# Optimization experiments

Hardware: AMD Instinct MI355X
Metric: run time of the kernel (lower is better)

Reference implementation:

```python
import jax, jax.numpy as jnp
import numpy as np

N_NODES = 4_000_000   # numNodes in the morphological tree
K_ATTRS = 6           # attributes per group
H = W = 4096          # image size
BETA_F = 100.0        # sigmoid gain (init kwarg)
N_DOUBLE = 22         # ceil(log2(N_NODES)) pointer-doubling steps


def setup_inputs() -> dict:
    key = jax.random.key(0)
    k1, k2, k3 = jax.random.split(key, 3)
    rng = np.random.default_rng(0)

    attrs2d = jax.random.uniform(k1, (N_NODES, K_ATTRS), dtype=jnp.float32)
    weight = jax.random.normal(k2, (K_ATTRS,), dtype=jnp.float32) * 0.5
    bias = jnp.zeros((1,), dtype=jnp.float32)
    # per-node gray-level residue (increment w.r.t. parent), non-negative for a max-tree
    residue = jax.random.uniform(k3, (N_NODES,), dtype=jnp.float32)

    # parent pointers: parent[i] < i (nodes in topological order), root 0 -> dummy node N
    par = np.empty(N_NODES + 1, dtype=np.int32)
    par[0] = N_NODES                       # root points at dummy
    idx = np.arange(1, N_NODES)
    par[1:N_NODES] = (rng.random(N_NODES - 1) * idx).astype(np.int32)
    par[N_NODES] = N_NODES                 # dummy is its own parent (value 0)
    parent = jnp.asarray(par)

    pixel_to_node = jnp.asarray(
        rng.integers(0, N_NODES, size=(H * W,), dtype=np.int32))

    return {"attrs2d": attrs2d, "weight": weight, "bias": bias,
            "residue": residue, "parent": parent, "pixel_to_node": pixel_to_node}


def _connected_filter(gate, residue, parent, pixel_to_node):
    """Soft connected filtering: y(p) = sum over root->node(p) path of gate*residue."""
    # append dummy node with value 0 at index N_NODES
    vals = jnp.concatenate([gate * residue, jnp.zeros((1,), gate.dtype)])  # (N+1,)
    cum, ptr = vals, parent
    for _ in range(N_DOUBLE):  # pointer doubling over the parent chain
        cum = cum + cum[ptr]
        ptr = ptr[ptr]
    return cum[pixel_to_node].reshape(H, W)


def reference(attrs2d, weight, bias, residue, parent, pixel_to_node):
    # logits = A @ w + b ; s = clamp(beta_f * logits, +-12) ; gate = sigmoid(s)
    logits = attrs2d @ weight + bias[0]                 # (N,)
    s = jnp.clip(BETA_F * logits, -12.0, 12.0)
    gate = jax.nn.sigmoid(s)
    return _connected_filter(gate, residue, parent, pixel_to_node)  # (H, W)
```

## Files before the change

### kernel.cpp

```cpp
#include <hip/hip_runtime.h>
#include <hip/hip_bf16.h>


typedef float v2f __attribute__((ext_vector_type(2)));
typedef float v4f __attribute__((ext_vector_type(4)));
typedef int   v4i __attribute__((ext_vector_type(4)));

#define NB 512
#define CHUNK_PX 8192
#define CV4 2048

__global__ __launch_bounds__(256) void k_gate_count512(
        const float* __restrict__ attrs, const float* __restrict__ w,
        const float* __restrict__ bias, const float* __restrict__ residue,
        const int* __restrict__ parent, int2* __restrict__ packed, int N,
        const int* __restrict__ ptn, unsigned short* __restrict__ wcnt,
        int shift, int g1) {
    __shared__ int hist[NB];
    if ((int)blockIdx.x >= g1) {
        int chunk = blockIdx.x - g1;
        int tid = threadIdx.x;
        for (int i = tid; i < NB; i += 256) hist[i] = 0;
        __syncthreads();
        const v4i* p4 = reinterpret_cast<const v4i*>(ptn) + (size_t)chunk * CV4;
        for (int t = 0; t < CV4/256; ++t) {
            v4i ia = __builtin_nontemporal_load(p4 + t*256 + tid);
            atomicAdd(&hist[ia.x >> shift], 1);
            atomicAdd(&hist[ia.y >> shift], 1);
            atomicAdd(&hist[ia.z >> shift], 1);
            atomicAdd(&hist[ia.w >> shift], 1);
        }
        __syncthreads();
        unsigned short* wc = wcnt + (size_t)chunk * NB;
        for (int i = tid; i < NB; i += 256) wc[i] = (unsigned short)hist[i];
        return;
    }
    int i = blockIdx.x * blockDim.x + threadIdx.x;
    if (i > N) return;
    if (i == N) { int2 p; p.x = N; p.y = __float_as_int(0.0f); packed[N] = p; return; }
    const v2f* a2 = reinterpret_cast<const v2f*>(attrs + (size_t)i * 6);
    v2f a0  = __builtin_nontemporal_load(a2 + 0);
    v2f a1  = __builtin_nontemporal_load(a2 + 1);
    v2f a2v = __builtin_nontemporal_load(a2 + 2);
    float logit = bias[0]
                + a0.x  * w[0] + a0.y  * w[1]
                + a1.x  * w[2] + a1.y  * w[3]
                + a2v.x * w[4] + a2v.y * w[5];
    float s = fminf(fmaxf(100.0f * logit, -12.0f), 12.0f);
    float gate = 1.0f / (1.0f + __expf(-s));
    float vv = gate * __builtin_nontemporal_load(residue + i);
    int2 p; p.x = __builtin_nontemporal_load(parent + i); p.y = __float_as_int(vv);
    packed[i] = p;
}

__global__ __launch_bounds__(512) void k_scanA(const unsigned short* __restrict__ wcnt,
                                               int* __restrict__ P) {
    int g = blockIdx.x, b = threadIdx.x;
    const unsigned short* base = wcnt + (size_t)g * 32 * NB;
    int s = 0;
    for (int i = 0; i < 32; ++i) s += base[(size_t)i*NB + b];
    P[(size_t)g*NB + b] = s;
}

__global__ __launch_bounds__(512) void k_scanB(int* __restrict__ P,
                                               int* __restrict__ binStart,
                                               int* __restrict__ binCnt, int nGroups) {
    int b = threadIdx.x, lane = b & 63, wave = b >> 6;
    int tot = 0;
    for (int g = 0; g < nGroups; ++g) {
        int t = P[(size_t)g*NB + b]; P[(size_t)g*NB + b] = tot; tot += t;
    }
    binCnt[b] = tot;
    int pad = (tot + 63) & ~63;
    int inc = pad;
    #pragma unroll
    for (int d = 1; d < 64; d <<= 1) { int o = __shfl_up(inc, d); if (lane >= d) inc += o; }
    __shared__ int wsum[8];
    if (lane == 63) wsum[wave] = inc;
    __syncthreads();
    int wb = 0;
    for (int ww = 0; ww < wave; ++ww) wb += wsum[ww];
    binStart[b] = wb + inc - pad;
}

__global__ __launch_bounds__(512) void k_scanC(const unsigned short* __restrict__ wcnt,
                                               const int* __restrict__ P,
                                               const int* __restrict__ binStart,
                                               int* __restrict__ bases) {
    int g = blockIdx.x, b = threadIdx.x;
    int run = binStart[b] + P[(size_t)g*NB + b];
    for (int i = 0; i < 32; ++i) {
        size_t c = (size_t)g*32 + i;
        bases[c*NB + b] = run;
        run += wcnt[c*NB + b];
    }
}

__global__ void k_walk_lvl0(const int2* __restrict__ packed,
                            float* __restrict__ cum, int hi, int N) {
    int i = blockIdx.x * blockDim.x + threadIdx.x;
    if (i >= hi) return;
    float s = 0.0f; int j = i;
    while (j != N) { int2 pv = packed[j]; s += __int_as_float(pv.y); j = pv.x; }
    cum[i] = s;
}

__global__ void k_walk_lvl(const int2* __restrict__ packed,
                           float* __restrict__ cum, int lo, int hi, int cutoff) {
    int i = lo + blockIdx.x * blockDim.x + threadIdx.x;
    if (i >= hi) return;
    float s = 0.0f; int j = i;
    do { int2 pv = packed[j]; s += __int_as_float(pv.y); j = pv.x; } while (j >= cutoff);
    cum[i] = s + cum[j];
}

__device__ __forceinline__ void exscan_bins(int* __restrict__ cnt,
                                            int* __restrict__ chEx,
                                            int* __restrict__ wsum) {
    int tid = threadIdx.x, lane = tid & 63, wave = tid >> 6;
    int b0 = 2*tid;
    int s0 = cnt[b0], s1 = cnt[b0+1], s = s0 + s1;
    int inc = s;
    #pragma unroll
    for (int d = 1; d < 64; d <<= 1) { int o = __shfl_up(inc, d); if (lane >= d) inc += o; }
    if (lane == 63) wsum[wave] = inc;
    __syncthreads();
    int wb = 0;
    for (int ww = 0; ww < wave; ++ww) wb += wsum[ww];
    int ex = wb + inc - s;
    chEx[b0] = ex; chEx[b0+1] = ex + s0;
}

__global__ __launch_bounds__(256) void k_scatter512(
        const int* __restrict__ ptn, const unsigned short* __restrict__ wcnt,
        const int* __restrict__ bases, int* __restrict__ nv,
        unsigned short* __restrict__ slotLocal, int shift) {
    __shared__ int cnt[NB];
    __shared__ int chEx[NB];
    __shared__ int alloc[NB];
    __shared__ int sbase[NB];
    __shared__ int ldss[CHUNK_PX];
    __shared__ int wsum[4];
    int chunk = blockIdx.x;
    int tid = threadIdx.x;
    const unsigned short* wc = wcnt + (size_t)chunk * NB;
    const int* bs = bases + (size_t)chunk * NB;
    for (int i = tid; i < NB; i += 256) { cnt[i] = wc[i]; sbase[i] = bs[i]; }
    __syncthreads();
    exscan_bins(cnt, chEx, wsum);
    __syncthreads();
    for (int i = tid; i < NB; i += 256) alloc[i] = chEx[i];
    __syncthreads();
    const v4i* p4 = reinterpret_cast<const v4i*>(ptn) + (size_t)chunk * CV4;
    unsigned long long* sl8 = reinterpret_cast<unsigned long long*>(slotLocal)
                              + (size_t)chunk * CV4;
    for (int t = 0; t < CV4/256; ++t) {
        v4i ia = __builtin_nontemporal_load(p4 + t*256 + tid);
        int s0 = atomicAdd(&alloc[ia.x >> shift], 1);
        int s1 = atomicAdd(&alloc[ia.y >> shift], 1);
        int s2 = atomicAdd(&alloc[ia.z >> shift], 1);
        int s3 = atomicAdd(&alloc[ia.w >> shift], 1);
        ldss[s0] = ia.x; ldss[s1] = ia.y; ldss[s2] = ia.z; ldss[s3] = ia.w;
        unsigned long long pk = (unsigned long long)(unsigned)s0
                              | ((unsigned long long)(unsigned)s1 << 16)
                              | ((unsigned long long)(unsigned)s2 << 32)
                              | ((unsigned long long)(unsigned)s3 << 48);
        sl8[t*256 + tid] = pk;
    }
    __syncthreads();
    {
        int grp = tid >> 4;
        int l16 = tid & 15;
        for (int b = grp; b < NB; b += 16) {
            int st = chEx[b], n = cnt[b], dst = sbase[b];
            for (int i = l16; i < n; i += 16)
                nv[dst + i] = ldss[st + i];
        }
    }
}

__global__ __launch_bounds__(512) void k_gather512(
        int* __restrict__ nv, const float* __restrict__ cum,
        const int* __restrict__ binStart, const int* __restrict__ binCnt,
        int shift, int N) {
    __shared__ float slice[8192];
    int b = blockIdx.x;
    int base = b << shift;
    int W = 1 << shift;
    for (int i = threadIdx.x; i < W; i += 512) {
        int idx = base + i;
        slice[i] = (idx < N) ? cum[idx] : 0.0f;
    }
    __syncthreads();
    int s = binStart[b], cnt = binCnt[b];
    int nq = cnt >> 2;
    v4i* np = reinterpret_cast<v4i*>(nv + s);
    v4f* vp = reinterpret_cast<v4f*>(nv + s);
    for (int q = threadIdx.x; q < nq; q += 512) {
        v4i na = __builtin_nontemporal_load(np + q);
        v4f va;
        va.x = slice[na.x - base];
        va.y = slice[na.y - base];
        va.z = slice[na.z - base];
        va.w = slice[na.w - base];
        vp[q] = va;
    }
    int r = cnt & 3;
    if ((int)threadIdx.x < r) {
        int i = s + nq*4 + threadIdx.x;
        float v = slice[nv[i] - base];
        reinterpret_cast<float*>(nv)[i] = v;
    }
}

__global__ __launch_bounds__(256) void k_merge512(
        const unsigned short* __restrict__ wcnt, const int* __restrict__ bases,
        const float* __restrict__ nvf, const unsigned short* __restrict__ slotLocal,
        float* __restrict__ out) {
    __shared__ int cnt[NB];
    __shared__ int chEx[NB + 1];
    __shared__ int sbase[NB];
    __shared__ float ldsv[CHUNK_PX];
    __shared__ int wsum[4];
    int chunk = blockIdx.x;
    int tid = threadIdx.x;
    const unsigned short* wc = wcnt + (size_t)chunk * NB;
    const int* bs = bases + (size_t)chunk * NB;
    for (int i = tid; i < NB; i += 256) { cnt[i] = wc[i]; sbase[i] = bs[i]; }
    __syncthreads();
    exscan_bins(cnt, chEx, wsum);
    if (tid == 0) chEx[NB] = CHUNK_PX;
    __syncthreads();
    {
        int grp = tid >> 4;
        int l16 = tid & 15;
        for (int b = grp; b < NB; b += 16) {
            int st = chEx[b], n = cnt[b], src = sbase[b];
            for (int i = l16; i < n; i += 16)
                ldsv[st + i] = nvf[src + i];
        }
    }
    __syncthreads();
    const unsigned long long* sl8 = reinterpret_cast<const unsigned long long*>(slotLocal)
                                    + (size_t)chunk * CV4;
    v4f* o4 = reinterpret_cast<v4f*>(out) + (size_t)chunk * CV4;
    for (int t = 0; t < CV4/256; ++t) {
        unsigned long long pk = __builtin_nontemporal_load(sl8 + t*256 + tid);
        v4f o;
        o.x = ldsv[pk & 0xFFFF];
        o.y = ldsv[(pk >> 16) & 0xFFFF];
        o.z = ldsv[(pk >> 32) & 0xFFFF];
        o.w = ldsv[(pk >> 48) & 0xFFFF];
        o4[t*256 + tid] = o;
    }
}

__global__ void k_pixel_gather(const float* __restrict__ cum,
                               const int* __restrict__ ptn,
                               float* __restrict__ out, int M) {
    int t = blockIdx.x * blockDim.x + threadIdx.x;
    int base = t * 4;
    if (base + 3 < M) {
        v4i idx = __builtin_nontemporal_load(reinterpret_cast<const v4i*>(ptn) + t);
        float4 o;
        o.x = cum[idx.x]; o.y = cum[idx.y]; o.z = cum[idx.z]; o.w = cum[idx.w];
        reinterpret_cast<float4*>(out)[t] = o;
    } else {
        for (int p = base; p < M; ++p) out[p] = cum[ptn[p]];
    }
}

extern "C" void kernel_launch(void* const* d_in, const int* in_sizes, int n_in,
                              void* d_out, int out_size, void* d_ws, size_t ws_size,
                              hipStream_t stream) {
    const float* attrs   = (const float*)d_in[0];
    const float* weight  = (const float*)d_in[1];
    const float* bias    = (const float*)d_in[2];
    const float* residue = (const float*)d_in[3];
    const int*   parent  = (const int*)d_in[4];
    const int*   ptn     = (const int*)d_in[5];
    float* out = (float*)d_out;

    const int N  = in_sizes[3];
    const int HW = in_sizes[5];
    const int BLK = 256;

    int shift = 0;
    while (((long)(N - 1) >> shift) >= NB) ++shift;
    int nBins = (int)(((long)(N - 1) >> shift) + 1);

    const int nChunks = HW / CHUNK_PX;
    const int nGroups = nChunks / 32;

    auto align256 = [](size_t x) { return (x + 255) & ~(size_t)255; };
    const size_t cumB   = align256((size_t)(N + 1) * 4);
    const size_t pkB    = (size_t)(N + 1) * 8;
    const size_t slB    = (size_t)HW * 2;
    const size_t regA   = align256(pkB > slB ? pkB : slB);
    const size_t nvB    = align256(((size_t)HW + (size_t)NB*64) * 4);
    const size_t wcntB  = align256((size_t)nChunks * NB * 2);
    const size_t PB     = align256((size_t)nGroups * NB * 4);
    const size_t basesB = align256((size_t)nChunks * NB * 4);
    const size_t need   = cumB + regA + nvB + wcntB + PB + basesB + 4096;

    float* cum    = (float*)d_ws;
    int2*  packed = (int2*)((char*)d_ws + cumB);
    unsigned short* slotLocal = (unsigned short*)((char*)d_ws + cumB);
    int*   nv     = (int*)((char*)d_ws + cumB + regA);
    unsigned short* wcnt = (unsigned short*)((char*)d_ws + cumB + regA + nvB);
    int*   P      = (int*)((char*)d_ws + cumB + regA + nvB + wcntB);
    int*   bases  = (int*)((char*)d_ws + cumB + regA + nvB + wcntB + PB);
    int*   binStart = (int*)((char*)d_ws + cumB + regA + nvB + wcntB + PB + basesB);
    int*   binCnt   = binStart + NB;

    bool binnedOK = (HW % CHUNK_PX == 0) && (nChunks % 32 == 0) && (nChunks >= 32) &&
                    (shift <= 13) && (ws_size >= need) && (N >= 2);

    int g1 = (N + 1 + BLK - 1) / BLK;
    int gC = binnedOK ? nChunks : 0;
    k_gate_count512<<<g1 + gC, BLK, 0, stream>>>(attrs, weight, bias, residue,
                                                 parent, packed, N,
                                                 ptn, wcnt, shift, g1);

    if (binnedOK) {
        k_scanA<<<nGroups, 512, 0, stream>>>(wcnt, P);
        k_scanB<<<1, 512, 0, stream>>>(P, binStart, binCnt, nGroups);
        k_scanC<<<nGroups, 512, 0, stream>>>(wcnt, P, binStart, bases);
    }

    int c0 = 16384;   if (c0 > N) c0 = N;
    int c1 = 262144;  if (c1 > N) c1 = N;
    int c2 = 1048576; if (c2 > N) c2 = N;

    k_walk_lvl0<<<(c0 + BLK - 1) / BLK, BLK, 0, stream>>>(packed, cum, c0, N);
    if (c1 > c0)
        k_walk_lvl<<<(c1 - c0 + BLK - 1) / BLK, BLK, 0, stream>>>(packed, cum, c0, c1, c0);
    if (c2 > c1)
        k_walk_lvl<<<(c2 - c1 + BLK - 1) / BLK, BLK, 0, stream>>>(packed, cum, c1, c2, c1);
    if (N > c2)
        k_walk_lvl<<<(N - c2 + BLK - 1) / BLK, BLK, 0, stream>>>(packed, cum, c2, N, c2);

    if (binnedOK) {
        k_scatter512<<<nChunks, BLK, 0, stream>>>(ptn, wcnt, bases, nv, slotLocal, shift);
        k_gather512<<<nBins, 512, 0, stream>>>(nv, cum, binStart, binCnt, shift, N);
        k_merge512<<<nChunks, BLK, 0, stream>>>(wcnt, bases, (const float*)nv,
                                                slotLocal, out);
    } else {
        int nQuads = (HW + 3) / 4;
        k_pixel_gather<<<(nQuads + BLK - 1) / BLK, BLK, 0, stream>>>(cum, ptn, out, HW);
    }
}
```

Baseline: 320.9 us.

## Interleave last-level tree walk with pixel scatter in one fused launch

The final pointer-walk level and the pixel scatter now run in a single interleaved kernel whose blocks alternate between scatter chunks and walk blocks. This lets the latency-bound walk overlap with the bandwidth-bound scatter instead of running them back to back. To make that safe, slotLocal moves to its own workspace region, because it previously aliased the packed buffer the walk reads. Chunk size is halved (4096 pixels) to double the number of chunks, and the bin-copy loops switch to 8-lane groups. Smaller chunks mean more per-chunk histogram and scan overhead and more, shorter bin runs.

```diff
diff --git a/kernel.cpp b/kernel.cpp
--- a/kernel.cpp
+++ b/kernel.cpp
@@ -7,8 +7,8 @@
 typedef int   v4i __attribute__((ext_vector_type(4)));
 
 #define NB 512
-#define CHUNK_PX 8192
-#define CV4 2048
+#define CHUNK_PX 4096
+#define CV4 1024
 
 __global__ __launch_bounds__(256) void k_gate_count512(
         const float* __restrict__ attrs, const float* __restrict__ w,
@@ -131,7 +131,7 @@
     chEx[b0] = ex; chEx[b0+1] = ex + s0;
 }
 
-__global__ __launch_bounds__(256) void k_scatter512(
+__device__ void scatter_chunk_body(int chunk,
         const int* __restrict__ ptn, const unsigned short* __restrict__ wcnt,
         const int* __restrict__ bases, int* __restrict__ nv,
         unsigned short* __restrict__ slotLocal, int shift) {
@@ -141,7 +141,6 @@
     __shared__ int sbase[NB];
     __shared__ int ldss[CHUNK_PX];
     __shared__ int wsum[4];
-    int chunk = blockIdx.x;
     int tid = threadIdx.x;
     const unsigned short* wc = wcnt + (size_t)chunk * NB;
     const int* bs = bases + (size_t)chunk * NB;
@@ -168,15 +167,41 @@
         sl8[t*256 + tid] = pk;
     }
     __syncthreads();
-    {
-        int grp = tid >> 4;
-        int l16 = tid & 15;
-        for (int b = grp; b < NB; b += 16) {
-            int st = chEx[b], n = cnt[b], dst = sbase[b];
-            for (int i = l16; i < n; i += 16)
-                nv[dst + i] = ldss[st + i];
-        }
-    }
+    int grp = tid >> 3;
+    int l8 = tid & 7;
+    for (int b = grp; b < NB; b += 32) {
+        int st = chEx[b], n = cnt[b], dst = sbase[b];
+        for (int i = l8; i < n; i += 8)
+            nv[dst + i] = ldss[st + i];
+    }
+}
+
+__global__ __launch_bounds__(256) void k_scatter512(
+        const int* __restrict__ ptn, const unsigned short* __restrict__ wcnt,
+        const int* __restrict__ bases, int* __restrict__ nv,
+        unsigned short* __restrict__ slotLocal, int shift) {
+    scatter_chunk_body(blockIdx.x, ptn, wcnt, bases, nv, slotLocal, shift);
+}
+
+__global__ __launch_bounds__(256) void k_walk3_scatter(
+        const int* __restrict__ ptn, const unsigned short* __restrict__ wcnt,
+        const int* __restrict__ bases, int* __restrict__ nv,
+        unsigned short* __restrict__ slotLocal, int shift, int gS, int k,
+        const int2* __restrict__ packed, float* __restrict__ cum,
+        int lo, int hi, int cutoff) {
+    int b = blockIdx.x;
+    int q = b / k, r = b - q * k;
+    if (r == 0 && q < gS) {
+        scatter_chunk_body(q, ptn, wcnt, bases, nv, slotLocal, shift);
+        return;
+    }
+    int nsb = (q < gS) ? (q + (r > 0 ? 1 : 0)) : gS;
+    int wIdx = b - nsb;
+    int i = lo + wIdx * 256 + threadIdx.x;
+    if (i >= hi) return;
+    float s = 0.0f; int j = i;
+    do { int2 pv = packed[j]; s += __int_as_float(pv.y); j = pv.x; } while (j >= cutoff);
+    cum[i] = s + cum[j];
 }
 
 __global__ __launch_bounds__(512) void k_gather512(
@@ -232,11 +257,11 @@
     if (tid == 0) chEx[NB] = CHUNK_PX;
     __syncthreads();
     {
-        int grp = tid >> 4;
-        int l16 = tid & 15;
-        for (int b = grp; b < NB; b += 16) {
+        int grp = tid >> 3;
+        int l8 = tid & 7;
+        for (int b = grp; b < NB; b += 32) {
             int st = chEx[b], n = cnt[b], src = sbase[b];
-            for (int i = l16; i < n; i += 16)
+            for (int i = l8; i < n; i += 8)
                 ldsv[st + i] = nvf[src + i];
         }
     }
@@ -301,11 +326,11 @@
     const size_t wcntB  = align256((size_t)nChunks * NB * 2);
     const size_t PB     = align256((size_t)nGroups * NB * 4);
     const size_t basesB = align256((size_t)nChunks * NB * 4);
-    const size_t need   = cumB + regA + nvB + wcntB + PB + basesB + 4096;
+    const size_t needSeq  = cumB + regA + nvB + wcntB + PB + basesB + 4096;
+    const size_t needIntl = needSeq + align256(slB);
 
     float* cum    = (float*)d_ws;
     int2*  packed = (int2*)((char*)d_ws + cumB);
-    unsigned short* slotLocal = (unsigned short*)((char*)d_ws + cumB);
     int*   nv     = (int*)((char*)d_ws + cumB + regA);
     unsigned short* wcnt = (unsigned short*)((char*)d_ws + cumB + regA + nvB);
     int*   P      = (int*)((char*)d_ws + cumB + regA + nvB + wcntB);
@@ -314,7 +339,11 @@
     int*   binCnt   = binStart + NB;
 
     bool binnedOK = (HW % CHUNK_PX == 0) && (nChunks % 32 == 0) && (nChunks >= 32) &&
-                    (shift <= 13) && (ws_size >= need) && (N >= 2);
+                    (shift <= 13) && (ws_size >= needSeq) && (N >= 2);
+    bool intl = binnedOK && (ws_size >= needIntl);
+    unsigned short* slotLocal = intl
+        ? (unsigned short*)((char*)d_ws + needSeq)
+        : (unsigned short*)((char*)d_ws + cumB);
 
     int g1 = (N + 1 + BLK - 1) / BLK;
     int gC = binnedOK ? nChunks : 0;
@@ -337,15 +366,27 @@
         k_walk_lvl<<<(c1 - c0 + BLK - 1) / BLK, BLK, 0, stream>>>(packed, cum, c0, c1, c0);
     if (c2 > c1)
         k_walk_lvl<<<(c2 - c1 + BLK - 1) / BLK, BLK, 0, stream>>>(packed, cum, c1, c2, c1);
-    if (N > c2)
-        k_walk_lvl<<<(N - c2 + BLK - 1) / BLK, BLK, 0, stream>>>(packed, cum, c2, N, c2);
 
     if (binnedOK) {
-        k_scatter512<<<nChunks, BLK, 0, stream>>>(ptn, wcnt, bases, nv, slotLocal, shift);
+        int gW3 = (N > c2) ? (N - c2 + BLK - 1) / BLK : 0;
+        if (intl && gW3 > 0) {
+            int G = gW3 + nChunks;
+            int k = G / nChunks;
+            k_walk3_scatter<<<G, BLK, 0, stream>>>(ptn, wcnt, bases, nv, slotLocal,
+                                                   shift, nChunks, k,
+                                                   packed, cum, c2, N, c2);
+        } else {
+            if (gW3 > 0)
+                k_walk_lvl<<<gW3, BLK, 0, stream>>>(packed, cum, c2, N, c2);
+            k_scatter512<<<nChunks, BLK, 0, stream>>>(ptn, wcnt, bases, nv,
+                                                      slotLocal, shift);
+        }
         k_gather512<<<nBins, 512, 0, stream>>>(nv, cum, binStart, binCnt, shift, N);
         k_merge512<<<nChunks, BLK, 0, stream>>>(wcnt, bases, (const float*)nv,
                                                 slotLocal, out);
     } else {
+        if (N > c2)
+            k_walk_lvl<<<(N - c2 + BLK - 1) / BLK, BLK, 0, stream>>>(packed, cum, c2, N, c2);
         int nQuads = (HW + 3) / 4;
         k_pixel_gather<<<(nQuads + BLK - 1) / BLK, BLK, 0, stream>>>(cum, ptn, out, HW);
     }
```

Measured after the change: 334.7 us. +4.3%, slower.
